# Kernel optimization log

Hardware: AMD Instinct MI355X
Metric: run time of the kernel (lower is better)

Reference implementation:

```python
import jax, jax.numpy as jnp
import numpy as np

RADIUS = 0.4
NSAMPLE = 32
EPS = 1e-5  # BatchNorm2d default eps


def setup_inputs() -> dict:
    key = jax.random.key(0)
    ks = jax.random.split(key, 16)
    B, N, C, P = 16, 4096, 128, 1024
    inp = {
        "xyz": jax.random.uniform(ks[0], (B, N, 3), dtype=jnp.float32),
        "features": jax.random.normal(ks[1], (B, C, N), dtype=jnp.float32),
        "num_points": P,
    }
    dims = [C + 3, 128, 128, 256]  # in_channel = mlps[0] + 3, then mlps[1:]
    for i in range(3):
        cin, cout = dims[i], dims[i + 1]
        inp[f"w{i}"] = jax.random.normal(ks[2 + 4 * i], (cout, cin), jnp.float32) * (1.0 / np.sqrt(cin))
        inp[f"b{i}"] = jnp.zeros((cout,), jnp.float32)
        inp[f"g{i}"] = jnp.ones((cout,), jnp.float32)
        inp[f"beta{i}"] = jnp.zeros((cout,), jnp.float32)
    return inp


def _ball_query_group(xyz, new_xyz, features):
    """QueryAndGroup: ball query (first NSAMPLE in-radius indices, padded with
    the first hit), gather, subtract center, concat [rel_xyz; feats]."""
    N = xyz.shape[1]
    # squared distances [B, P, N]
    d2 = jnp.sum((new_xyz[:, :, None, :] - xyz[:, None, :, :]) ** 2, axis=-1)
    cand = jnp.where(d2 < RADIUS * RADIUS,
                     jnp.arange(N, dtype=jnp.int32)[None, None, :], N)
    idx = jnp.sort(cand, axis=-1)[:, :, :NSAMPLE]          # first hits, in order
    idx = jnp.where(idx == N, idx[:, :, :1], idx)           # pad with first hit
    # gather per batch: xyz [N,3] indexed by idx [P,S] -> [P,S,3]
    grouped_xyz = jax.vmap(lambda p, i: p[i])(xyz, idx) - new_xyz[:, :, None, :]
    # features [C,N] indexed along N -> [C,P,S]
    grouped_feat = jax.vmap(lambda f, i: f[:, i])(features, idx)
    # [B, 3+C, P, S]
    return jnp.concatenate([grouped_xyz.transpose(0, 3, 1, 2), grouped_feat], axis=1), idx


def _conv_bn_relu(x, w, b, g, beta):
    # 1x1 Conv2d: pointwise channel mix over [B, Cin, P, S]
    x = jnp.einsum('oi,bips->bops', w, x) + b[None, :, None, None]
    # BatchNorm2d, training mode (batch statistics over B,P,S per channel)
    m = jnp.mean(x, axis=(0, 2, 3), keepdims=True)
    v = jnp.mean((x - m) ** 2, axis=(0, 2, 3), keepdims=True)
    x = g[None, :, None, None] * (x - m) * jax.lax.rsqrt(v + EPS) + beta[None, :, None, None]
    return jax.nn.relu(x)


def reference(xyz, features, num_points,
              w0, b0, g0, beta0, w1, b1, g1, beta1, w2, b2, g2, beta2):
    B = xyz.shape[0]
    # use_fps=False: sample_idxs = arange(num_points) per batch
    sample_idxs = jnp.tile(jnp.arange(num_points, dtype=jnp.int32)[None], (B, 1))
    new_xyz = xyz[:, :num_points]                    # gather_operation with arange
    x, _ = _ball_query_group(xyz, new_xyz, features)  # [B, 131, P, S]
    for w, b, g, bt in ((w0, b0, g0, beta0), (w1, b1, g1, beta1), (w2, b2, g2, beta2)):
        x = _conv_bn_relu(x, w, b, g, bt)
    new_features = jnp.max(x, axis=-1)               # max-pool over nsample
    return new_xyz, new_features, sample_idxs
```

## Files before the change

kernel.cpp:

```cpp
#include <hip/hip_runtime.h>

#define BB 16
#define NN 4096
#define CC 128
#define PP 1024
#define SS 32
#define MM (BB*PP*SS)
#define NBLK 8192
#define OFF_NF 49152
#define OFF_SI 4243456

typedef unsigned short u16;
typedef unsigned int u32;
typedef __attribute__((ext_vector_type(8))) short short8v;
typedef __attribute__((ext_vector_type(4))) float f32x4;

__device__ __forceinline__ float b2f(u16 u) {
    union { float f; unsigned i; } x; x.i = ((unsigned)u) << 16; return x.f;
}
__device__ __forceinline__ u16 f2b(float f) {
    union { float f; unsigned i; } x; x.f = f;
    unsigned r = x.i + 0x7fffu + ((x.i >> 16) & 1u);
    return (u16)(r >> 16);
}
__device__ __forceinline__ float2 act2(u32 u, float2 s0, float2 s1) {
    union { float f; unsigned i; } a, b;
    a.i = u << 16; b.i = u & 0xffff0000u;
    return make_float2(fmaxf(fmaf(s0.x, a.f, s0.y), 0.f),
                       fmaxf(fmaf(s1.x, b.f, s1.y), 0.f));
}
__device__ __forceinline__ u32 packbf(float flo, float fhi) {
    union { float f; unsigned i; } x0, x1; x0.f = flo; x1.f = fhi;
    return __builtin_amdgcn_perm(x1.i, x0.i, 0x07060302u);
}
__device__ __forceinline__ u32 packbf_rtne(float flo, float fhi) {
    union { float f; unsigned i; } x0, x1; x0.f = flo; x1.f = fhi;
    u32 r0 = x0.i + 0x7fffu + ((x0.i >> 16) & 1u);
    u32 r1 = x1.i + 0x7fffu + ((x1.i >> 16) & 1u);
    return __builtin_amdgcn_perm(r1, r0, 0x07060302u);
}
__device__ __forceinline__ u32 act_pack(u32 u, float2 s0, float2 s1) {
    float2 f = act2(u, s0, s1);
    return packbf(f.x, f.y);
}
__device__ __forceinline__ short8v as_s8(uint4 v) {
    union { uint4 u; short8v s; } x; x.u = v; return x.s;
}

#define MFMA16(a,b,c) __builtin_amdgcn_mfma_f32_16x16x32_bf16(a,b,c,0,0,0)

__global__ void k_init(const float* __restrict__ xyz, const float* __restrict__ w0,
                       const float* __restrict__ w1, const float* __restrict__ w2,
                       float* __restrict__ out, float* __restrict__ w0t,
                       u16* __restrict__ w0b, u16* __restrict__ w1b,
                       u16* __restrict__ w2b) {
    int i = blockIdx.x * 256 + threadIdx.x;
    if (i < 49152) {
        int b = i / 3072, r = i % 3072;
        out[i] = xyz[b * 12288 + r];
        return;
    }
    int j = i - 49152;
    if (j < 16384) { out[OFF_SI + j] = (float)(j & 1023); return; }
    int e = j - 16384;
    if (e < 384) { w0t[e] = w0[(e & 127) * 131 + (e >> 7)]; return; }
    int f = e - 384;
    if (f < 16384) { w0b[f] = f2b(w0[(f >> 7) * 131 + 3 + (f & 127)]); return; }
    int h = f - 16384;
    if (h < 16384) { w1b[h] = f2b(w1[h]); return; }
    int k2 = h - 16384;
    if (k2 < 32768) { w2b[k2] = f2b(w2[k2]); }
}

__global__ __launch_bounds__(256) void k_ballquery(const float* __restrict__ xyz,
                                                   int* __restrict__ oidx,
                                                   float* __restrict__ relx,
                                                   float* __restrict__ rely,
                                                   float* __restrict__ relz) {
    __shared__ float sx[NN], sy[NN], sz[NN];
    int t = threadIdx.x, w = t >> 6, lane = t & 63;
    int b = blockIdx.x >> 8;
    int p = (blockIdx.x & 255) * 4 + w;
    const float* xb = xyz + (long)b * NN * 3;
    for (int i = t; i < NN; i += 256) {
        sx[i] = xb[3 * i]; sy[i] = xb[3 * i + 1]; sz[i] = xb[3 * i + 2];
    }
    __syncthreads();
    const float R2 = (float)(0.4 * 0.4);
    float cx = sx[p], cy = sy[p], cz = sz[p];
    int o = (b * PP + p) * SS;
    int cnt = 0, firstn = 0;
    float fdx = 0.f, fdy = 0.f, fdz = 0.f;
    for (int c = 0; c < 64 && cnt < 32; ++c) {
        int n = c * 64 + lane;
        float dx = __fsub_rn(sx[n], cx);
        float dy = __fsub_rn(sy[n], cy);
        float dz = __fsub_rn(sz[n], cz);
        float d2 = __fadd_rn(__fadd_rn(__fmul_rn(dx, dx), __fmul_rn(dy, dy)),
                             __fmul_rn(dz, dz));
        bool hit = d2 < R2;
        unsigned long long mask = __ballot(hit);
        if (mask) {
            if (cnt == 0) {
                int fl = __ffsll(mask) - 1;
                firstn = c * 64 + fl;
                fdx = __shfl(dx, fl); fdy = __shfl(dy, fl); fdz = __shfl(dz, fl);
            }
            int pos = cnt + __popcll(mask & ((1ull << lane) - 1ull));
            if (hit && pos < 32) {
                oidx[o + pos] = n;
                relx[o + pos] = dx; rely[o + pos] = dy; relz[o + pos] = dz;
            }
            cnt += __popcll(mask);
        }
    }
    if (lane < 32 && lane >= cnt) {
        oidx[o + lane] = firstn;
        relx[o + lane] = fdx; rely[o + lane] = fdy; relz[o + lane] = fdz;
    }
}

__global__ __launch_bounds__(256) void k_f1(const float* __restrict__ feat,
                                            const u16* __restrict__ w0b,
                                            float* __restrict__ F1) {
    __shared__ uint4 abuf[64 * 17];
    int t = threadIdx.x;
    int w = t >> 6, lane = t & 63, q = lane >> 4, l16 = lane & 15;
    int cb = (w & 1) * 64, wm0 = (w >> 1) * 32;
    short8v bf[4][4];
#pragma unroll
    for (int ct = 0; ct < 4; ++ct)
#pragma unroll
        for (int k0 = 0; k0 < 4; ++k0)
            bf[ct][k0] = *(const short8v*)(w0b + (cb + ct * 16 + l16) * 128 + k0 * 32 + q * 8);
    int nl = t & 63, cg = t >> 6;
    const float* fcol = feat + (long)(blockIdx.x >> 6) * (128 * 4096)
                             + (long)(blockIdx.x & 63) * 64 + nl;
#pragma unroll
    for (int pp = 0; pp < 4; ++pp) {
        int oct = cg + 4 * pp;
        float v[8];
#pragma unroll
        for (int r = 0; r < 8; ++r) v[r] = fcol[(long)(oct * 8 + r) * 4096];
        uint4 ov;
        ov.x = packbf_rtne(v[0], v[1]); ov.y = packbf_rtne(v[2], v[3]);
        ov.z = packbf_rtne(v[4], v[5]); ov.w = packbf_rtne(v[6], v[7]);
        abuf[nl * 17 + ((oct + nl) & 15)] = ov;
    }
    __syncthreads();
    f32x4 acc[2][4];
#pragma unroll
    for (int mt = 0; mt < 2; ++mt)
#pragma unroll
        for (int ct = 0; ct < 4; ++ct) acc[mt][ct] = (f32x4){0.f, 0.f, 0.f, 0.f};
#pragma unroll
    for (int mt = 0; mt < 2; ++mt) {
        int row = wm0 + mt * 16 + l16;
#pragma unroll
        for (int k0 = 0; k0 < 4; ++k0) {
            uint4 vv = abuf[row * 17 + ((k0 * 4 + q + row) & 15)];
            short8v af = as_s8(vv);
#pragma unroll
            for (int ct = 0; ct < 4; ++ct)
                acc[mt][ct] = MFMA16(af, bf[ct][k0], acc[mt][ct]);
        }
    }
    long nbase = (long)blockIdx.x * 64;
#pragma unroll
    for (int mt = 0; mt < 2; ++mt)
#pragma unroll
        for (int ct = 0; ct < 4; ++ct)
#pragma unroll
            for (int r = 0; r < 4; ++r)
                F1[(nbase + wm0 + mt * 16 + q * 4 + r) * 128 + cb + ct * 16 + l16]
                    = acc[mt][ct][r];
}

__global__ __launch_bounds__(256) void k_y0(const float* __restrict__ relx,
                                            const float* __restrict__ rely,
                                            const float* __restrict__ relz,
                                            const float* __restrict__ w0t,
                                            const float* __restrict__ F1,
                                            const int* __restrict__ idx,
                                            u16* __restrict__ y0,
                                            float* __restrict__ part,
                                            float* __restrict__ partq) {
    int t = threadIdx.x, w = t >> 6, lane = t & 63;
    long m0 = (long)blockIdx.x * 64;
    int c0 = 2 * lane;
    float wx0 = w0t[c0],       wx1 = w0t[c0 + 1];
    float wy0 = w0t[128 + c0], wy1 = w0t[128 + c0 + 1];
    float wz0 = w0t[256 + c0], wz1 = w0t[256 + c0 + 1];
    float s1a = 0.f, s1b = 0.f, s2a = 0.f, s2b = 0.f;
    u32* yo = (u32*)y0;
#pragma unroll 4
    for (int i = 0; i < 16; ++i) {
        long m = m0 + w + 4 * i;
        int b = (int)(m >> 15);
        int id = idx[m];
        float rx = relx[m], ry = rely[m], rz = relz[m];
        float2 f = *(const float2*)(F1 + ((long)(b * NN + id)) * 128 + c0);
        float v0 = fmaf(wx0, rx, fmaf(wy0, ry, fmaf(wz0, rz, f.x)));
        float v1 = fmaf(wx1, rx, fmaf(wy1, ry, fmaf(wz1, rz, f.y)));
        yo[m * 64 + lane] = packbf_rtne(v0, v1);
        s1a += v0; s2a = fmaf(v0, v0, s2a);
        s1b += v1; s2b = fmaf(v1, v1, s2b);
    }
    __shared__ float r1[128][4], r2[128][4];
    r1[c0][w] = s1a; r1[c0 + 1][w] = s1b;
    r2[c0][w] = s2a; r2[c0 + 1][w] = s2b;
    __syncthreads();
    if (t < 128) {
        float a1 = r1[t][0] + r1[t][1] + r1[t][2] + r1[t][3];
        float a2 = r2[t][0] + r2[t][1] + r2[t][2] + r2[t][3];
        part [(long)t * NBLK + blockIdx.x] = a1;
        partq[(long)t * NBLK + blockIdx.x] = a2;
    }
}

__global__ void k_bnfin(const float* __restrict__ part, const float* __restrict__ partq,
                        const float* __restrict__ g, const float* __restrict__ beta,
                        float* __restrict__ st, int nblk) {
    int co = blockIdx.x, t = threadIdx.x;
    const float* p1 = part + (long)co * NBLK;
    const float* p2 = partq + (long)co * NBLK;
    float s1 = 0.f, s2 = 0.f;
    for (int j = t; j < nblk; j += 256) { s1 += p1[j]; s2 += p2[j]; }
    __shared__ float r1[256], r2[256];
    r1[t] = s1; r2[t] = s2; __syncthreads();
    for (int off = 128; off > 0; off >>= 1) {
        if (t < off) { r1[t] += r1[t + off]; r2[t] += r2[t + off]; }
        __syncthreads();
    }
    if (t == 0) {
        const float inv = 1.f / (float)MM;
        float mean = r1[0] * inv;
        float var = r2[0] * inv - mean * mean;
        float sc = g[co] * rsqrtf(var + 1e-5f);
        st[2 * co] = sc;
        st[2 * co + 1] = fmaf(-mean, sc, beta[co]);
    }
}

__global__ __launch_bounds__(256, 3) void k_conv1(u16* __restrict__ y,
                                                  const u16* __restrict__ w1b,
                                                  const float* __restrict__ st0,
                                                  float* __restrict__ part,
                                                  float* __restrict__ partq) {
    __shared__ uint4 abuf[2][64 * 17];
    __shared__ float2 sst[128];
    __shared__ float sredA[4][64], sredB[4][64];
    int t = threadIdx.x;
    if (t < 128) sst[t] = ((const float2*)st0)[t];
    int w = t >> 6, lane = t & 63, q = lane >> 4, l16 = lane & 15;
    int wm0 = (w >> 1) * 32, cb = (w & 1) * 64;
    short8v bf[4][4];
#pragma unroll
    for (int ct = 0; ct < 4; ++ct)
#pragma unroll
        for (int k0 = 0; k0 < 4; ++k0)
            bf[ct][k0] = *(const short8v*)(w1b + (cb + ct * 16 + l16) * 128 + k0 * 32 + q * 8);
    __syncthreads();
    long m0b = (long)blockIdx.x * 512;
    float s1[4] = {0.f, 0.f, 0.f, 0.f}, s2[4] = {0.f, 0.f, 0.f, 0.f};
    int sr = t >> 4, sc16 = t & 15;
    for (int c = 0; c < 8; ++c) {
        long m0 = m0b + c * 64;
        uint4* ab = abuf[c & 1];
        const uint4* gsrc = (const uint4*)y;
#pragma unroll
        for (int p = 0; p < 4; ++p) {
            int r = p * 16 + sr;
            uint4 d = gsrc[(m0 + r) * 16 + sc16];
            uint4 o;
            o.x = act_pack(d.x, sst[sc16 * 8 + 0], sst[sc16 * 8 + 1]);
            o.y = act_pack(d.y, sst[sc16 * 8 + 2], sst[sc16 * 8 + 3]);
            o.z = act_pack(d.z, sst[sc16 * 8 + 4], sst[sc16 * 8 + 5]);
            o.w = act_pack(d.w, sst[sc16 * 8 + 6], sst[sc16 * 8 + 7]);
            ab[r * 17 + ((sc16 + r) & 15)] = o;
        }
        __syncthreads();
        f32x4 acc[2][4];
#pragma unroll
        for (int mt = 0; mt < 2; ++mt)
#pragma unroll
            for (int ct = 0; ct < 4; ++ct) acc[mt][ct] = (f32x4){0.f, 0.f, 0.f, 0.f};
#pragma unroll
        for (int mt = 0; mt < 2; ++mt) {
            int row = wm0 + mt * 16 + l16;
#pragma unroll
            for (int k0 = 0; k0 < 4; ++k0) {
                uint4 v = ab[row * 17 + ((k0 * 4 + q + row) & 15)];
                short8v af = as_s8(v);
#pragma unroll
                for (int ct = 0; ct < 4; ++ct)
                    acc[mt][ct] = MFMA16(af, bf[ct][k0], acc[mt][ct]);
            }
        }
#pragma unroll
        for (int mt = 0; mt < 2; ++mt)
#pragma unroll
            for (int ct = 0; ct < 4; ++ct)
#pragma unroll
                for (int r = 0; r < 4; ++r) {
                    float v = acc[mt][ct][r];
                    y[(m0 + wm0 + mt * 16 + q * 4 + r) * 128 + cb + ct * 16 + l16] = f2b(v);
                    s1[ct] += v; s2[ct] = fmaf(v, v, s2[ct]);
                }
    }
#pragma unroll
    for (int ct = 0; ct < 4; ++ct) {
        float a = s1[ct], b = s2[ct];
        a += __shfl_xor(a, 16); a += __shfl_xor(a, 32);
        b += __shfl_xor(b, 16); b += __shfl_xor(b, 32);
        if (lane < 16) { sredA[w][ct * 16 + l16] = a; sredB[w][ct * 16 + l16] = b; }
    }
    __syncthreads();
    if (t < 128) {
        int h = t >> 6, cl = t & 63;
        part [(long)t * NBLK + blockIdx.x] = sredA[h][cl] + sredA[h + 2][cl];
        partq[(long)t * NBLK + blockIdx.x] = sredB[h][cl] + sredB[h + 2][cl];
    }
}

__global__ __launch_bounds__(256) void k_conv2pool(const u16* __restrict__ y1,
                                                   const u16* __restrict__ w2b,
                                                   const float* __restrict__ st1,
                                                   float* __restrict__ rawmax,
                                                   float* __restrict__ rawmin,
                                                   float* __restrict__ part,
                                                   float* __restrict__ partq) {
    __shared__ uint4 abuf[2][64 * 17];
    __shared__ float2 sst[128];
    __shared__ float sredA[4][64], sredB[4][64];
    int t = threadIdx.x;
    if (t < 128) sst[t] = ((const float2*)st1)[t];
    int w = t >> 6, lane = t & 63, q = lane >> 4, l16 = lane & 15;
    int cb = w * 64;
    short8v bf[4][4];
#pragma unroll
    for (int ct = 0; ct < 4; ++ct)
#pragma unroll
        for (int k0 = 0; k0 < 4; ++k0)
            bf[ct][k0] = *(const short8v*)(w2b + (cb + ct * 16 + l16) * 128 + k0 * 32 + q * 8);
    __syncthreads();
    long m0b = (long)blockIdx.x * 512;
    int sr = t >> 4, sc16 = t & 15;
    float s1[4] = {0.f, 0.f, 0.f, 0.f}, s2[4] = {0.f, 0.f, 0.f, 0.f};
    for (int c = 0; c < 8; ++c) {
        long m0 = m0b + c * 64;
        uint4* ab = abuf[c & 1];
        const uint4* gsrc = (const uint4*)y1;
#pragma unroll
        for (int p = 0; p < 4; ++p) {
            int r = p * 16 + sr;
            uint4 d = gsrc[(m0 + r) * 16 + sc16];
            uint4 o;
            o.x = act_pack(d.x, sst[sc16 * 8 + 0], sst[sc16 * 8 + 1]);
            o.y = act_pack(d.y, sst[sc16 * 8 + 2], sst[sc16 * 8 + 3]);
            o.z = act_pack(d.z, sst[sc16 * 8 + 4], sst[sc16 * 8 + 5]);
            o.w = act_pack(d.w, sst[sc16 * 8 + 6], sst[sc16 * 8 + 7]);
            ab[r * 17 + ((sc16 + r) & 15)] = o;
        }
        __syncthreads();
        f32x4 acc[4][4];
#pragma unroll
        for (int mt = 0; mt < 4; ++mt)
#pragma unroll
            for (int ct = 0; ct < 4; ++ct) acc[mt][ct] = (f32x4){0.f, 0.f, 0.f, 0.f};
#pragma unroll
        for (int mt = 0; mt < 4; ++mt) {
            int row = mt * 16 + l16;
#pragma unroll
            for (int k0 = 0; k0 < 4; ++k0) {
                uint4 v = ab[row * 17 + ((k0 * 4 + q + row) & 15)];
                short8v af = as_s8(v);
#pragma unroll
                for (int ct = 0; ct < 4; ++ct)
                    acc[mt][ct] = MFMA16(af, bf[ct][k0], acc[mt][ct]);
            }
        }
#pragma unroll
        for (int ct = 0; ct < 4; ++ct) {
#pragma unroll
            for (int g = 0; g < 2; ++g) {
                f32x4 a0 = acc[2 * g][ct], a1 = acc[2 * g + 1][ct];
                s1[ct] += a0[0] + a0[1] + a0[2] + a0[3] + a1[0] + a1[1] + a1[2] + a1[3];
                s2[ct] = fmaf(a0[0], a0[0], s2[ct]); s2[ct] = fmaf(a0[1], a0[1], s2[ct]);
                s2[ct] = fmaf(a0[2], a0[2], s2[ct]); s2[ct] = fmaf(a0[3], a0[3], s2[ct]);
                s2[ct] = fmaf(a1[0], a1[0], s2[ct]); s2[ct] = fmaf(a1[1], a1[1], s2[ct]);
                s2[ct] = fmaf(a1[2], a1[2], s2[ct]); s2[ct] = fmaf(a1[3], a1[3], s2[ct]);
                float mx = fmaxf(fmaxf(fmaxf(a0[0], a0[1]), fmaxf(a0[2], a0[3])),
                                 fmaxf(fmaxf(a1[0], a1[1]), fmaxf(a1[2], a1[3])));
                float mn = fminf(fminf(fminf(a0[0], a0[1]), fminf(a0[2], a0[3])),
                                 fminf(fminf(a1[0], a1[1]), fminf(a1[2], a1[3])));
                mx = fmaxf(mx, __shfl_xor(mx, 16)); mx = fmaxf(mx, __shfl_xor(mx, 32));
                mn = fminf(mn, __shfl_xor(mn, 16)); mn = fminf(mn, __shfl_xor(mn, 32));
                if (lane < 16) {
                    long bp = (long)blockIdx.x * 16 + c * 2 + g;
                    rawmax[bp * 256 + cb + ct * 16 + l16] = mx;
                    rawmin[bp * 256 + cb + ct * 16 + l16] = mn;
                }
            }
        }
    }
#pragma unroll
    for (int ct = 0; ct < 4; ++ct) {
        float a = s1[ct], b = s2[ct];
        a += __shfl_xor(a, 16); a += __shfl_xor(a, 32);
        b += __shfl_xor(b, 16); b += __shfl_xor(b, 32);
        if (lane < 16) { sredA[w][ct * 16 + l16] = a; sredB[w][ct * 16 + l16] = b; }
    }
    __syncthreads();
    {
        part [(long)t * NBLK + blockIdx.x] = sredA[t >> 6][t & 63];
        partq[(long)t * NBLK + blockIdx.x] = sredB[t >> 6][t & 63];
    }
}

__global__ void k_final(const float* __restrict__ rawmax, const float* __restrict__ rawmin,
                        const float* __restrict__ st2, float* __restrict__ out) {
    __shared__ float tile[32][33];
    int b = blockIdx.x >> 8;
    int p0 = ((blockIdx.x >> 3) & 31) * 32;
    int c0 = (blockIdx.x & 7) * 32;
    int j = threadIdx.x & 31, i0 = threadIdx.x >> 5;
    float sc = st2[2 * (c0 + j)], sh = st2[2 * (c0 + j) + 1];
#pragma unroll
    for (int rr = 0; rr < 4; ++rr) {
        int i = i0 + rr * 8;
        long idx = ((long)(b * 1024 + p0 + i)) * 256 + c0 + j;
        float v = sc > 0.f ? fmaf(sc, rawmax[idx], sh) : fmaf(sc, rawmin[idx], sh);
        tile[i][j] = fmaxf(v, 0.f);
    }
    __syncthreads();
#pragma unroll
    for (int rr = 0; rr < 4; ++rr) {
        int i = i0 + rr * 8;
        out[OFF_NF + (long)b * 262144 + (c0 + i) * 1024 + p0 + j] = tile[j][i];
    }
}

extern "C" void kernel_launch(void* const* d_in, const int* in_sizes, int n_in,
                              void* d_out, int out_size, void* d_ws, size_t ws_size,
                              hipStream_t stream) {
    (void)in_sizes; (void)n_in; (void)out_size; (void)ws_size;
    const float* xyz  = (const float*)d_in[0];
    const float* feat = (const float*)d_in[1];
    const float* w0   = (const float*)d_in[3];
    const float* g0   = (const float*)d_in[5];
    const float* be0  = (const float*)d_in[6];
    const float* w1   = (const float*)d_in[7];
    const float* g1   = (const float*)d_in[9];
    const float* be1  = (const float*)d_in[10];
    const float* w2   = (const float*)d_in[11];
    const float* g2   = (const float*)d_in[13];
    const float* be2  = (const float*)d_in[14];
    float* out = (float*)d_out;

    char* ws = (char*)d_ws;
    size_t off = 0;
    auto alloc = [&](size_t bytes) -> void* {
        void* p = ws + off;
        off = (off + bytes + 4095) & ~(size_t)4095;
        return p;
    };
    int*   idx    = (int*)  alloc((size_t)MM * 4);
    float* relx   = (float*)alloc((size_t)MM * 4);
    float* rely   = (float*)alloc((size_t)MM * 4);
    float* relz   = (float*)alloc((size_t)MM * 4);
    float* w0t    = (float*)alloc(3 * 128 * 4);
    u16*   w0b    = (u16*)  alloc(128 * 128 * 2);
    u16*   w1b    = (u16*)  alloc(128 * 128 * 2);
    u16*   w2b    = (u16*)  alloc(256 * 128 * 2);
    float* st0    = (float*)alloc(128 * 2 * 4);
    float* st1    = (float*)alloc(128 * 2 * 4);
    float* st2    = (float*)alloc(256 * 2 * 4);
    float* part   = (float*)alloc((size_t)256 * NBLK * 4);
    float* partq  = (float*)alloc((size_t)256 * NBLK * 4);
    float* F1     = (float*)alloc((size_t)BB * NN * 128 * 4);
    float* rawmax = (float*)alloc((size_t)BB * PP * 256 * 4);
    float* rawmin = (float*)alloc((size_t)BB * PP * 256 * 4);
    u16*   bufA   = (u16*)  alloc((size_t)MM * 128 * 2);

    k_init<<<514, 256, 0, stream>>>(xyz, w0, w1, w2, out, w0t, w0b, w1b, w2b);
    k_ballquery<<<4096, 256, 0, stream>>>(xyz, idx, relx, rely, relz);
    k_f1<<<1024, 256, 0, stream>>>(feat, w0b, F1);
    k_y0<<<NBLK, 256, 0, stream>>>(relx, rely, relz, w0t, F1, idx, bufA, part, partq);
    k_bnfin<<<128, 256, 0, stream>>>(part, partq, g0, be0, st0, NBLK);
    k_conv1<<<1024, 256, 0, stream>>>(bufA, w1b, st0, part, partq);
    k_bnfin<<<128, 256, 0, stream>>>(part, partq, g1, be1, st1, 1024);
    k_conv2pool<<<1024, 256, 0, stream>>>(bufA, w2b, st1, rawmax, rawmin, part, partq);
    k_bnfin<<<256, 256, 0, stream>>>(part, partq, g2, be2, st2, 1024);
    k_final<<<4096, 256, 0, stream>>>(rawmax, rawmin, st2, out);
}
```

Measured before the change: 327.7 us.

## Recompute layer-0 activations in conv1 instead of storing bf16 y0

Ball query now writes packed float4 records (rel xyz + index bits) instead of four separate arrays. The y0 kernel becomes a stats-only pass with four times as many rows per block and no bf16 output. conv1 regathers F1 rows and recomputes the layer-0 pre-activation, then applies BN+ReLU directly into shared memory. This removes a 128-channel bf16 write and read of the full MM-row activation tensor, at the cost of doing the F1 gather and FMA work twice.

```diff
diff --git a/kernel.cpp b/kernel.cpp
--- a/kernel.cpp
+++ b/kernel.cpp
@@ -73,10 +73,7 @@
 }
 
 __global__ __launch_bounds__(256) void k_ballquery(const float* __restrict__ xyz,
-                                                   int* __restrict__ oidx,
-                                                   float* __restrict__ relx,
-                                                   float* __restrict__ rely,
-                                                   float* __restrict__ relz) {
+                                                   float4* __restrict__ rel4) {
     __shared__ float sx[NN], sy[NN], sz[NN];
     int t = threadIdx.x, w = t >> 6, lane = t & 63;
     int b = blockIdx.x >> 8;
@@ -108,15 +105,13 @@
             }
             int pos = cnt + __popcll(mask & ((1ull << lane) - 1ull));
             if (hit && pos < 32) {
-                oidx[o + pos] = n;
-                relx[o + pos] = dx; rely[o + pos] = dy; relz[o + pos] = dz;
+                rel4[o + pos] = make_float4(dx, dy, dz, __int_as_float(n));
             }
             cnt += __popcll(mask);
         }
     }
     if (lane < 32 && lane >= cnt) {
-        oidx[o + lane] = firstn;
-        relx[o + lane] = fdx; rely[o + lane] = fdy; relz[o + lane] = fdz;
+        rel4[o + lane] = make_float4(fdx, fdy, fdz, __int_as_float(firstn));
     }
 }
 
@@ -176,33 +171,27 @@
                     = acc[mt][ct][r];
 }
 
-__global__ __launch_bounds__(256) void k_y0(const float* __restrict__ relx,
-                                            const float* __restrict__ rely,
-                                            const float* __restrict__ relz,
-                                            const float* __restrict__ w0t,
-                                            const float* __restrict__ F1,
-                                            const int* __restrict__ idx,
-                                            u16* __restrict__ y0,
-                                            float* __restrict__ part,
-                                            float* __restrict__ partq) {
+__global__ __launch_bounds__(256) void k_y0stats(const float4* __restrict__ rel4,
+                                                 const float* __restrict__ w0t,
+                                                 const float* __restrict__ F1,
+                                                 float* __restrict__ part,
+                                                 float* __restrict__ partq) {
     int t = threadIdx.x, w = t >> 6, lane = t & 63;
-    long m0 = (long)blockIdx.x * 64;
     int c0 = 2 * lane;
     float wx0 = w0t[c0],       wx1 = w0t[c0 + 1];
     float wy0 = w0t[128 + c0], wy1 = w0t[128 + c0 + 1];
     float wz0 = w0t[256 + c0], wz1 = w0t[256 + c0 + 1];
+    int m0 = blockIdx.x * 256;
     float s1a = 0.f, s1b = 0.f, s2a = 0.f, s2b = 0.f;
-    u32* yo = (u32*)y0;
 #pragma unroll 4
-    for (int i = 0; i < 16; ++i) {
-        long m = m0 + w + 4 * i;
-        int b = (int)(m >> 15);
-        int id = idx[m];
-        float rx = relx[m], ry = rely[m], rz = relz[m];
-        float2 f = *(const float2*)(F1 + ((long)(b * NN + id)) * 128 + c0);
-        float v0 = fmaf(wx0, rx, fmaf(wy0, ry, fmaf(wz0, rz, f.x)));
-        float v1 = fmaf(wx1, rx, fmaf(wy1, ry, fmaf(wz1, rz, f.y)));
-        yo[m * 64 + lane] = packbf_rtne(v0, v1);
+    for (int i = 0; i < 64; ++i) {
+        int m = m0 + w + 4 * i;
+        float4 qv = rel4[m];
+        int id = __float_as_int(qv.w);
+        int b = m >> 15;
+        float2 f = *(const float2*)(F1 + ((long)(b * NN + id) << 7) + c0);
+        float v0 = fmaf(wx0, qv.x, fmaf(wy0, qv.y, fmaf(wz0, qv.z, f.x)));
+        float v1 = fmaf(wx1, qv.x, fmaf(wy1, qv.y, fmaf(wz1, qv.z, f.y)));
         s1a += v0; s2a = fmaf(v0, v0, s2a);
         s1b += v1; s2b = fmaf(v1, v1, s2b);
     }
@@ -242,16 +231,17 @@
     }
 }
 
-__global__ __launch_bounds__(256, 3) void k_conv1(u16* __restrict__ y,
+__global__ __launch_bounds__(256, 3) void k_conv1(const float4* __restrict__ rel4,
+                                                  const float* __restrict__ F1,
                                                   const u16* __restrict__ w1b,
+                                                  const float* __restrict__ w0t,
                                                   const float* __restrict__ st0,
+                                                  u16* __restrict__ y,
                                                   float* __restrict__ part,
                                                   float* __restrict__ partq) {
-    __shared__ uint4 abuf[2][64 * 17];
-    __shared__ float2 sst[128];
+    __shared__ u32 abuf[2][64 * 17 * 4];
     __shared__ float sredA[4][64], sredB[4][64];
     int t = threadIdx.x;
-    if (t < 128) sst[t] = ((const float2*)st0)[t];
     int w = t >> 6, lane = t & 63, q = lane >> 4, l16 = lane & 15;
     int wm0 = (w >> 1) * 32, cb = (w & 1) * 64;
     short8v bf[4][4];
@@ -260,24 +250,31 @@
 #pragma unroll
         for (int k0 = 0; k0 < 4; ++k0)
             bf[ct][k0] = *(const short8v*)(w1b + (cb + ct * 16 + l16) * 128 + k0 * 32 + q * 8);
-    __syncthreads();
-    long m0b = (long)blockIdx.x * 512;
+    int c0 = 2 * lane;
+    float wx0 = w0t[c0],       wx1 = w0t[c0 + 1];
+    float wy0 = w0t[128 + c0], wy1 = w0t[128 + c0 + 1];
+    float wz0 = w0t[256 + c0], wz1 = w0t[256 + c0 + 1];
+    float4 s4 = *(const float4*)(st0 + 2 * c0);
+    int m0b = blockIdx.x * 512;
     float s1[4] = {0.f, 0.f, 0.f, 0.f}, s2[4] = {0.f, 0.f, 0.f, 0.f};
-    int sr = t >> 4, sc16 = t & 15;
+    int rbase = w * 16;
+    int cg = lane >> 2, wsel = lane & 3;
     for (int c = 0; c < 8; ++c) {
-        long m0 = m0b + c * 64;
-        uint4* ab = abuf[c & 1];
-        const uint4* gsrc = (const uint4*)y;
-#pragma unroll
-        for (int p = 0; p < 4; ++p) {
-            int r = p * 16 + sr;
-            uint4 d = gsrc[(m0 + r) * 16 + sc16];
-            uint4 o;
-            o.x = act_pack(d.x, sst[sc16 * 8 + 0], sst[sc16 * 8 + 1]);
-            o.y = act_pack(d.y, sst[sc16 * 8 + 2], sst[sc16 * 8 + 3]);
-            o.z = act_pack(d.z, sst[sc16 * 8 + 4], sst[sc16 * 8 + 5]);
-            o.w = act_pack(d.w, sst[sc16 * 8 + 6], sst[sc16 * 8 + 7]);
-            ab[r * 17 + ((sc16 + r) & 15)] = o;
+        int m0 = m0b + c * 64;
+        u32* ab = abuf[c & 1];
+#pragma unroll
+        for (int j = 0; j < 16; ++j) {
+            int r = rbase + j;
+            int m = m0 + r;
+            float4 qv = rel4[m];
+            int id = __float_as_int(qv.w);
+            int b = m >> 15;
+            float2 f = *(const float2*)(F1 + ((long)(b * NN + id) << 7) + c0);
+            float v0 = fmaf(wx0, qv.x, fmaf(wy0, qv.y, fmaf(wz0, qv.z, f.x)));
+            float v1 = fmaf(wx1, qv.x, fmaf(wy1, qv.y, fmaf(wz1, qv.z, f.y)));
+            float a0 = fmaxf(fmaf(s4.x, v0, s4.y), 0.f);
+            float a1 = fmaxf(fmaf(s4.z, v1, s4.w), 0.f);
+            ab[(r * 17 + ((cg + r) & 15)) * 4 + wsel] = packbf(a0, a1);
         }
         __syncthreads();
         f32x4 acc[2][4];
@@ -285,12 +282,13 @@
         for (int mt = 0; mt < 2; ++mt)
 #pragma unroll
             for (int ct = 0; ct < 4; ++ct) acc[mt][ct] = (f32x4){0.f, 0.f, 0.f, 0.f};
+        const uint4* ab4 = (const uint4*)ab;
 #pragma unroll
         for (int mt = 0; mt < 2; ++mt) {
             int row = wm0 + mt * 16 + l16;
 #pragma unroll
             for (int k0 = 0; k0 < 4; ++k0) {
-                uint4 v = ab[row * 17 + ((k0 * 4 + q + row) & 15)];
+                uint4 v = ab4[row * 17 + ((k0 * 4 + q + row) & 15)];
                 short8v af = as_s8(v);
 #pragma unroll
                 for (int ct = 0; ct < 4; ++ct)
@@ -465,10 +463,7 @@
         off = (off + bytes + 4095) & ~(size_t)4095;
         return p;
     };
-    int*   idx    = (int*)  alloc((size_t)MM * 4);
-    float* relx   = (float*)alloc((size_t)MM * 4);
-    float* rely   = (float*)alloc((size_t)MM * 4);
-    float* relz   = (float*)alloc((size_t)MM * 4);
+    float4* rel4  = (float4*)alloc((size_t)MM * 16);
     float* w0t    = (float*)alloc(3 * 128 * 4);
     u16*   w0b    = (u16*)  alloc(128 * 128 * 2);
     u16*   w1b    = (u16*)  alloc(128 * 128 * 2);
@@ -484,11 +479,11 @@
     u16*   bufA   = (u16*)  alloc((size_t)MM * 128 * 2);
 
     k_init<<<514, 256, 0, stream>>>(xyz, w0, w1, w2, out, w0t, w0b, w1b, w2b);
-    k_ballquery<<<4096, 256, 0, stream>>>(xyz, idx, relx, rely, relz);
+    k_ballquery<<<4096, 256, 0, stream>>>(xyz, rel4);
     k_f1<<<1024, 256, 0, stream>>>(feat, w0b, F1);
-    k_y0<<<NBLK, 256, 0, stream>>>(relx, rely, relz, w0t, F1, idx, bufA, part, partq);
-    k_bnfin<<<128, 256, 0, stream>>>(part, partq, g0, be0, st0, NBLK);
-    k_conv1<<<1024, 256, 0, stream>>>(bufA, w1b, st0, part, partq);
+    k_y0stats<<<2048, 256, 0, stream>>>(rel4, w0t, F1, part, partq);
+    k_bnfin<<<128, 256, 0, stream>>>(part, partq, g0, be0, st0, 2048);
+    k_conv1<<<1024, 256, 0, stream>>>(rel4, F1, w1b, w0t, st0, bufA, part, partq);
     k_bnfin<<<128, 256, 0, stream>>>(part, partq, g1, be1, st1, 1024);
     k_conv2pool<<<1024, 256, 0, stream>>>(bufA, w2b, st1, rawmax, rawmin, part, partq);
     k_bnfin<<<256, 256, 0, stream>>>(part, partq, g2, be2, st2, 1024);
```

Result: slower. 364.4 us (+11.2%).
